# Kernel optimization log

Measured on AMD Instinct MI355X. Metric: run time of the kernel, lower is better.

Reference implementation:

```python
import jax, jax.numpy as jnp
import numpy as np

N = 50000      # nodes
E = 1_600_000  # edges
IN, HID, OUT, NC = 384, 128, 64, 2
EPS = 1e-5


def layer_norm(x, g, b):
    mu = x.mean(-1, keepdims=True)
    v = ((x - mu) ** 2).mean(-1, keepdims=True)
    return (x - mu) / jnp.sqrt(v + EPS) * g + b


def gat_conv(x, src, dst, ea, W, a_s, a_d, We, a_e, bias, n):
    """PyG GATConv, heads=1, edge_dim=1, add_self_loops with fill_value='mean'."""
    h = x @ W  # [n, F]
    # self-loop edge_attr = mean of incoming edge_attr per destination node
    ones = jnp.ones((src.shape[0],), h.dtype)
    cnt = jax.ops.segment_sum(ones, dst, num_segments=n)
    esum = jax.ops.segment_sum(ea, dst, num_segments=n)
    loop_ea = esum / jnp.maximum(cnt, 1.0)[:, None]
    loop = jnp.arange(n)
    s2 = jnp.concatenate([src, loop])
    d2 = jnp.concatenate([dst, loop])
    ea2 = jnp.concatenate([ea, loop_ea], axis=0)
    al_s = h @ a_s          # [n]
    al_d = h @ a_d          # [n]
    al_e = (ea2 @ We) @ a_e  # [E+n]
    logits = jax.nn.leaky_relu(al_s[s2] + al_d[d2] + al_e, 0.2)
    m = jax.ops.segment_max(logits, d2, num_segments=n)  # every node has a self loop
    ex = jnp.exp(logits - m[d2])
    den = jax.ops.segment_sum(ex, d2, num_segments=n)
    alpha = ex / den[d2]
    out = jax.ops.segment_sum(alpha[:, None] * h[s2], d2, num_segments=n)
    return out + bias


def setup_inputs() -> dict:
    key = jax.random.key(0)
    ks = jax.random.split(key, 20)
    def xav(k, fan_in, fan_out):
        s = float(np.sqrt(6.0 / (fan_in + fan_out)))
        return jax.random.uniform(k, (fan_in, fan_out), jnp.float32, -s, s)
    x = jax.random.normal(ks[0], (N, IN), jnp.float32)
    edge_index = jax.random.randint(ks[1], (2, E), 0, N)
    edge_attr = jax.random.normal(ks[2], (E, 1), jnp.float32)
    return {
        "x": x, "edge_index": edge_index, "edge_attr": edge_attr,
        "ln1_g": jnp.ones((IN,), jnp.float32), "ln1_b": jnp.zeros((IN,), jnp.float32),
        "fc1_w": xav(ks[3], IN, HID), "fc1_b": jnp.zeros((HID,), jnp.float32),
        "conv1_w": xav(ks[4], HID, HID),
        "conv1_as": jax.random.normal(ks[5], (HID,), jnp.float32) * 0.1,
        "conv1_ad": jax.random.normal(ks[6], (HID,), jnp.float32) * 0.1,
        "conv1_we": xav(ks[7], 1, HID),
        "conv1_ae": jax.random.normal(ks[8], (HID,), jnp.float32) * 0.1,
        "conv1_b": jnp.zeros((HID,), jnp.float32),
        "conv2_w": xav(ks[9], HID, OUT),
        "conv2_as": jax.random.normal(ks[10], (OUT,), jnp.float32) * 0.1,
        "conv2_ad": jax.random.normal(ks[11], (OUT,), jnp.float32) * 0.1,
        "conv2_we": xav(ks[12], 1, OUT),
        "conv2_ae": jax.random.normal(ks[13], (OUT,), jnp.float32) * 0.1,
        "conv2_b": jnp.zeros((OUT,), jnp.float32),
        "ln2_g": jnp.ones((OUT,), jnp.float32), "ln2_b": jnp.zeros((OUT,), jnp.float32),
        "fc2_w": xav(ks[14], OUT, NC), "fc2_b": jnp.zeros((NC,), jnp.float32),
    }


def reference(x, edge_index, edge_attr,
              ln1_g, ln1_b, fc1_w, fc1_b,
              conv1_w, conv1_as, conv1_ad, conv1_we, conv1_ae, conv1_b,
              conv2_w, conv2_as, conv2_ad, conv2_we, conv2_ae, conv2_b,
              ln2_g, ln2_b, fc2_w, fc2_b):
    src, dst = edge_index[0], edge_index[1]
    n = x.shape[0]
    h = layer_norm(x, ln1_g, ln1_b) @ fc1_w + fc1_b
    h = gat_conv(h, src, dst, edge_attr, conv1_w, conv1_as, conv1_ad, conv1_we, conv1_ae, conv1_b, n)
    h = jax.nn.leaky_relu(h, 0.01)
    h = gat_conv(h, src, dst, edge_attr, conv2_w, conv2_as, conv2_ad, conv2_we, conv2_ae, conv2_b, n)
    h = jax.nn.leaky_relu(h, 0.01)
    out = layer_norm(h, ln2_g, ln2_b) @ fc2_w + fc2_b
    return out
```

## Files before the change

### kernel.cpp

```cpp
#include <hip/hip_runtime.h>

#define NN 50000
#define NE 1600000
#define CAP 64
#define NBIN 196
#define NBLK 391
#define RUNCAP 48

typedef __attribute__((ext_vector_type(8))) short short8v;
typedef __attribute__((ext_vector_type(4))) float f32x4;

__device__ __forceinline__ float wsum(float v) {
#pragma unroll
  for (int m = 32; m > 0; m >>= 1) v += __shfl_xor(v, m, 64);
  return v;
}
__device__ __forceinline__ float wmax(float v) {
#pragma unroll
  for (int m = 32; m > 0; m >>= 1) v = fmaxf(v, __shfl_xor(v, m, 64));
  return v;
}
__device__ __forceinline__ float leakyf(float x, float s) { return x > 0.f ? x : s * x; }

__device__ __forceinline__ unsigned short bfr(float f) {
  unsigned u = __float_as_uint(f);
  return (unsigned short)((u + 0x7FFFu + ((u >> 16) & 1u)) >> 16);
}
__device__ __forceinline__ unsigned pack2(float a, float b) {
  return (unsigned)bfr(a) | ((unsigned)bfr(b) << 16);
}
__device__ __forceinline__ float bflo(unsigned u) { return __uint_as_float(u << 16); }
__device__ __forceinline__ float bfhi(unsigned u) { return __uint_as_float(u & 0xFFFF0000u); }

__global__ __launch_bounds__(256) void k_bin1(const int* __restrict__ src,
                                              const int* __restrict__ dst,
                                              const float* __restrict__ ea,
                                              int2* __restrict__ binRun,
                                              int* __restrict__ runLen) {
  __shared__ int cur[NBIN];
  int tid = threadIdx.x, b = blockIdx.x;
  for (int i = tid; i < NBIN; i += 256) cur[i] = 0;
  __syncthreads();
  int2* myRun = binRun + (size_t)b * NBIN * RUNCAP;
  int base4 = b * 1024;
#pragma unroll
  for (int i = 0; i < 4; ++i) {
    int t4 = base4 + i * 256 + tid;
    if (t4 < NE / 4) {
      int4 s = ((const int4*)src)[t4];
      int4 d = ((const int4*)dst)[t4];
      float4 a = ((const float4*)ea)[t4];
      int bin, p;
      bin = d.x >> 8; p = atomicAdd(&cur[bin], 1);
      if (p < RUNCAP) myRun[bin * RUNCAP + p] = make_int2(s.x | ((d.x & 255) << 16), __float_as_int(a.x));
      bin = d.y >> 8; p = atomicAdd(&cur[bin], 1);
      if (p < RUNCAP) myRun[bin * RUNCAP + p] = make_int2(s.y | ((d.y & 255) << 16), __float_as_int(a.y));
      bin = d.z >> 8; p = atomicAdd(&cur[bin], 1);
      if (p < RUNCAP) myRun[bin * RUNCAP + p] = make_int2(s.z | ((d.z & 255) << 16), __float_as_int(a.z));
      bin = d.w >> 8; p = atomicAdd(&cur[bin], 1);
      if (p < RUNCAP) myRun[bin * RUNCAP + p] = make_int2(s.w | ((d.w & 255) << 16), __float_as_int(a.w));
    }
  }
  __syncthreads();
  for (int i = tid; i < NBIN; i += 256) runLen[b * NBIN + i] = min(cur[i], RUNCAP);
}

__global__ __launch_bounds__(256) void k_bin2(const int2* __restrict__ binRun,
                                              const int* __restrict__ runLen,
                                              int2* __restrict__ edat, int* __restrict__ cnt) {
  __shared__ int cur[256];
  __shared__ int rl[NBLK];
  int tid = threadIdx.x, j = blockIdx.x;
  cur[tid] = 0;
  for (int i = tid; i < NBLK; i += 256) rl[i] = runLen[i * NBIN + j];
  __syncthreads();
  const int TOT = NBLK * RUNCAP;
  for (int g = tid; g < TOT; g += 256) {
    int b = g / RUNCAP, r = g - b * RUNCAP;
    if (r < rl[b]) {
      int2 rec = binRun[(size_t)b * NBIN * RUNCAP + j * RUNCAP + r];
      int srcv = rec.x & 0xFFFF;
      int dlow = rec.x >> 16;
      int dstv = (j << 8) | dlow;
      int p = atomicAdd(&cur[dlow], 1);
      if (p < CAP) edat[(size_t)dstv * CAP + p] = make_int2(srcv, rec.y);
    }
  }
  __syncthreads();
  int dstv = (j << 8) | tid;
  if (dstv < NN) cnt[dstv] = min(cur[tid], CAP);
}

__global__ void k_prep(const float* __restrict__ W, const float* __restrict__ g,
                       const float* __restrict__ b, const float* __restrict__ fb,
                       const float* __restrict__ we1, const float* __restrict__ ae1,
                       const float* __restrict__ we2, const float* __restrict__ ae2,
                       float* __restrict__ u, float* __restrict__ v, float* __restrict__ ce) {
  __shared__ float r1[128], r2[128];
  int c = threadIdx.x;
  float ua = 0.f, va = 0.f;
#pragma unroll 4
  for (int k = 0; k < 384; ++k) {
    float w = W[k * 128 + c];
    ua += g[k] * w;
    va += b[k] * w;
  }
  u[c] = ua;
  v[c] = va + fb[c];
  r1[c] = we1[c] * ae1[c];
  r2[c] = (c < 64) ? we2[c] * ae2[c] : 0.f;
  __syncthreads();
  for (int o = 64; o > 0; o >>= 1) {
    if (c < o) { r1[c] += r1[c + o]; r2[c] += r2[c + o]; }
    __syncthreads();
  }
  if (c == 0) { ce[0] = r1[0]; ce[1] = r2[0]; }
}

__global__ void k_prepT(const float* __restrict__ W1, const float* __restrict__ g,
                        const float* __restrict__ cw1, const float* __restrict__ cw2,
                        unsigned short* __restrict__ WgF, unsigned short* __restrict__ W1F,
                        unsigned short* __restrict__ W2F) {
  int tid = blockIdx.x * 256 + threadIdx.x;
  int stride = gridDim.x * 256;
  for (int i = tid; i < 8 * 12 * 512; i += stride) {
    int j = i & 7, lane = (i >> 3) & 63, tk = i >> 9;
    int ks = tk % 12, t = tk / 12;
    int c = t * 16 + (lane & 15);
    int k = ks * 32 + (lane >> 4) * 8 + j;
    WgF[i] = bfr(g[k] * W1[k * 128 + c]);
  }
  for (int i = tid; i < 8 * 4 * 512; i += stride) {
    int j = i & 7, lane = (i >> 3) & 63, tk = i >> 9;
    int ks = tk & 3, t = tk >> 2;
    int c = t * 16 + (lane & 15);
    int k = ks * 32 + (lane >> 4) * 8 + j;
    W1F[i] = bfr(cw1[k * 128 + c]);
  }
  for (int i = tid; i < 4 * 4 * 512; i += stride) {
    int j = i & 7, lane = (i >> 3) & 63, tk = i >> 9;
    int ks = tk & 3, t = tk >> 2;
    int c = t * 16 + (lane & 15);
    int k = ks * 32 + (lane >> 4) * 8 + j;
    W2F[i] = bfr(cw2[k * 64 + c]);
  }
}

__global__ __launch_bounds__(256) void k_fc1_h1(
    const float* __restrict__ x, const unsigned short* __restrict__ WgF,
    const unsigned short* __restrict__ W1F, const float* __restrict__ u,
    const float* __restrict__ v, const float* __restrict__ a_s,
    const float* __restrict__ a_d, unsigned short* __restrict__ Hb,
    float* __restrict__ al_s, float* __restrict__ al_d) {
  __shared__ __align__(16) unsigned short xs[64][392];
  __shared__ float mu_s[64], rs_s[64];
  int tid = threadIdx.x, wv = tid >> 6, lane = tid & 63;
  int lrow = lane & 15, lk = lane >> 4;
  long n0 = (long)blockIdx.x * 64;
  for (int rr = 0; rr < 16; ++rr) {
    int r = wv * 16 + rr;
    long gr = n0 + r;
    if (gr > NN - 1) gr = NN - 1;
    const float* xr = x + gr * 384;
    float s = 0.f, ss = 0.f;
#pragma unroll
    for (int js = 0; js < 3; ++js) {
      float2 val = *(const float2*)&xr[lane * 2 + 128 * js];
      s += val.x + val.y;
      ss += val.x * val.x + val.y * val.y;
      *(unsigned*)&xs[r][lane * 2 + 128 * js] = pack2(val.x, val.y);
    }
    s = wsum(s);
    ss = wsum(ss);
    if (lane == 0) {
      float mu = s * (1.f / 384.f);
      float var = ss * (1.f / 384.f) - mu * mu;
      mu_s[r] = mu;
      rs_s[r] = rsqrtf(var + 1e-5f);
    }
  }
  __syncthreads();
  const unsigned short* abase = &xs[wv * 16 + lrow][lk * 8];
  f32x4 acc[8] = {};
  for (int ks = 0; ks < 12; ++ks) {
    short8v A = *(const short8v*)(abase + ks * 32);
#pragma unroll
    for (int t = 0; t < 8; ++t) {
      short8v B = *(const short8v*)&WgF[((t * 12 + ks) * 64 + lane) * 8];
      acc[t] = __builtin_amdgcn_mfma_f32_16x16x32_bf16(A, B, acc[t], 0, 0, 0);
    }
  }
  float uc[8], vc[8];
#pragma unroll
  for (int t = 0; t < 8; ++t) {
    int c = t * 16 + lrow;
    uc[t] = u[c];
    vc[t] = v[c];
  }
#pragma unroll
  for (int reg = 0; reg < 4; ++reg) {
    int rl = wv * 16 + lk * 4 + reg;
    float mu = mu_s[rl], rs = rs_s[rl];
#pragma unroll
    for (int t = 0; t < 8; ++t) {
      float val = rs * (acc[t][reg] - mu * uc[t]) + vc[t];
      xs[rl][t * 16 + lrow] = bfr(val);
    }
  }
  __syncthreads();
  f32x4 acc2[8] = {};
#pragma unroll
  for (int ks = 0; ks < 4; ++ks) {
    short8v A = *(const short8v*)(abase + ks * 32);
#pragma unroll
    for (int t = 0; t < 8; ++t) {
      short8v B = *(const short8v*)&W1F[((t * 4 + ks) * 64 + lane) * 8];
      acc2[t] = __builtin_amdgcn_mfma_f32_16x16x32_bf16(A, B, acc2[t], 0, 0, 0);
    }
  }
  float asv[8], adv[8];
#pragma unroll
  for (int t = 0; t < 8; ++t) {
    asv[t] = a_s[t * 16 + lrow];
    adv[t] = a_d[t * 16 + lrow];
  }
#pragma unroll
  for (int reg = 0; reg < 4; ++reg) {
    float ps = 0.f, pd = 0.f;
#pragma unroll
    for (int t = 0; t < 8; ++t) {
      ps += acc2[t][reg] * asv[t];
      pd += acc2[t][reg] * adv[t];
    }
#pragma unroll
    for (int m = 1; m < 16; m <<= 1) {
      ps += __shfl_xor(ps, m, 64);
      pd += __shfl_xor(pd, m, 64);
    }
    long rg = n0 + wv * 16 + lk * 4 + reg;
    if (rg < NN) {
      if (lrow == 0) { al_s[rg] = ps; al_d[rg] = pd; }
#pragma unroll
      for (int t = 0; t < 8; ++t) Hb[rg * 128 + t * 16 + lrow] = bfr(acc2[t][reg]);
    }
  }
}

template <int NT>
__global__ __launch_bounds__(256) void k_mxw(
    const unsigned short* __restrict__ Xb, const unsigned short* __restrict__ WF,
    const float* __restrict__ a_s, const float* __restrict__ a_d,
    unsigned short* __restrict__ Hb, float* __restrict__ al_s, float* __restrict__ al_d) {
  __shared__ __align__(16) unsigned short xs[64][136];
  int tid = threadIdx.x, wv = tid >> 6, lane = tid & 63;
  int lrow = lane & 15, lk = lane >> 4;
  long n0 = (long)blockIdx.x * 64;
  for (int rr = 0; rr < 16; ++rr) {
    int r = wv * 16 + rr;
    long gr = n0 + r;
    if (gr > NN - 1) gr = NN - 1;
    *(unsigned*)&xs[r][lane * 2] = *(const unsigned*)&Xb[gr * 128 + lane * 2];
  }
  __syncthreads();
  const unsigned short* abase = &xs[wv * 16 + lrow][lk * 8];
  f32x4 acc[NT] = {};
#pragma unroll
  for (int ks = 0; ks < 4; ++ks) {
    short8v A = *(const short8v*)(abase + ks * 32);
#pragma unroll
    for (int t = 0; t < NT; ++t) {
      short8v B = *(const short8v*)&WF[((t * 4 + ks) * 64 + lane) * 8];
      acc[t] = __builtin_amdgcn_mfma_f32_16x16x32_bf16(A, B, acc[t], 0, 0, 0);
    }
  }
  float asv[NT], adv[NT];
#pragma unroll
  for (int t = 0; t < NT; ++t) {
    asv[t] = a_s[t * 16 + lrow];
    adv[t] = a_d[t * 16 + lrow];
  }
#pragma unroll
  for (int reg = 0; reg < 4; ++reg) {
    float ps = 0.f, pd = 0.f;
#pragma unroll
    for (int t = 0; t < NT; ++t) {
      ps += acc[t][reg] * asv[t];
      pd += acc[t][reg] * adv[t];
    }
#pragma unroll
    for (int m = 1; m < 16; m <<= 1) {
      ps += __shfl_xor(ps, m, 64);
      pd += __shfl_xor(pd, m, 64);
    }
    long rg = n0 + wv * 16 + lk * 4 + reg;
    if (rg < NN) {
      if (lrow == 0) { al_s[rg] = ps; al_d[rg] = pd; }
#pragma unroll
      for (int t = 0; t < NT; ++t) Hb[rg * (NT * 16) + t * 16 + lrow] = bfr(acc[t][reg]);
    }
  }
}

template <int F, bool OB, bool FUSE_LN>
__global__ __launch_bounds__(256) void k_agg(
    const unsigned short* __restrict__ Hb, const float* __restrict__ al_s,
    const float* __restrict__ al_d, const float* __restrict__ cep,
    const int* __restrict__ cntA, const int2* __restrict__ edat,
    const float* __restrict__ bias, void* __restrict__ outp,
    const float* __restrict__ g2, const float* __restrict__ b2,
    const float* __restrict__ w2, const float* __restrict__ fb2) {
  int wv = threadIdx.x >> 6, lane = threadIdx.x & 63;
  int i = blockIdx.x * 4 + wv;
  int cnt = min(cntA[i], CAP);
  float ce = *cep;
  float ald = al_d[i];
  bool valid = lane < cnt;
  int s = 0;
  float eav = 0.f, lg = -1e30f;
  if (valid) {
    int2 ed = edat[(size_t)i * CAP + lane];
    s = ed.x;
    eav = __int_as_float(ed.y);
    lg = leakyf(al_s[s] + ald + ce * eav, 0.2f);
  }
  float easum = wsum(eav);
  float loop_ea = easum / fmaxf((float)cnt, 1.f);
  float lg_self = leakyf(al_s[i] + ald + ce * loop_ea, 0.2f);
  float mx = fmaxf(wmax(lg), lg_self);
  float e = valid ? __expf(lg - mx) : 0.f;
  float es_ = __expf(lg_self - mx);
  float den = wsum(e) + es_;
  float acc0, acc1 = 0.f;
  if (F == 128) {
    unsigned u = *(const unsigned*)&Hb[(size_t)i * 128 + 2 * lane];
    acc0 = es_ * bflo(u);
    acc1 = es_ * bfhi(u);
  } else {
    acc0 = es_ * __uint_as_float(((unsigned)Hb[(size_t)i * 64 + lane]) << 16);
  }
  int t = 0;
  for (; t + 8 <= cnt; t += 8) {
    float et[8];
    unsigned uu[8];
#pragma unroll
    for (int j = 0; j < 8; ++j) {
      et[j] = __shfl(e, t + j, 64);
      int sj = __shfl(s, t + j, 64);
      if (F == 128)
        uu[j] = *(const unsigned*)&Hb[(size_t)sj * 128 + 2 * lane];
      else
        uu[j] = ((unsigned)Hb[(size_t)sj * 64 + lane]) << 16;
    }
#pragma unroll
    for (int j = 0; j < 8; ++j) {
      if (F == 128) {
        acc0 += et[j] * bflo(uu[j]);
        acc1 += et[j] * bfhi(uu[j]);
      } else {
        acc0 += et[j] * __uint_as_float(uu[j]);
      }
    }
  }
  for (; t < cnt; ++t) {
    float et = __shfl(e, t, 64);
    int st = __shfl(s, t, 64);
    if (F == 128) {
      unsigned u = *(const unsigned*)&Hb[(size_t)st * 128 + 2 * lane];
      acc0 += et * bflo(u);
      acc1 += et * bfhi(u);
    } else {
      acc0 += et * __uint_as_float(((unsigned)Hb[(size_t)st * 64 + lane]) << 16);
    }
  }
  float inv = 1.f / den;
  if (F == 128) {
    float2 bv = *(const float2*)&bias[2 * lane];
    float o0 = leakyf(acc0 * inv + bv.x, 0.01f);
    float o1 = leakyf(acc1 * inv + bv.y, 0.01f);
    if (OB) {
      ((unsigned*)outp)[(size_t)i * 64 + lane] = pack2(o0, o1);
    } else {
      *(float2*)&((float*)outp)[(size_t)i * 128 + 2 * lane] = make_float2(o0, o1);
    }
  } else {
    float o = leakyf(acc0 * inv + bias[lane], 0.01f);
    if (FUSE_LN) {
      float sum = wsum(o);
      float ssum = wsum(o * o);
      float mu = sum * (1.f / 64.f);
      float var = ssum * (1.f / 64.f) - mu * mu;
      float rs = rsqrtf(var + 1e-5f);
      float xn = (o - mu) * rs * g2[lane] + b2[lane];
      float q0 = wsum(xn * w2[lane * 2 + 0]);
      float q1 = wsum(xn * w2[lane * 2 + 1]);
      if (lane == 0) {
        ((float*)outp)[(size_t)i * 2 + 0] = q0 + fb2[0];
        ((float*)outp)[(size_t)i * 2 + 1] = q1 + fb2[1];
      }
    } else {
      ((float*)outp)[(size_t)i * 64 + lane] = o;
    }
  }
}

extern "C" void kernel_launch(void* const* d_in, const int* in_sizes, int n_in,
                              void* d_out, int out_size, void* d_ws, size_t ws_size,
                              hipStream_t stream) {
  const int N = NN;
  const float* x = (const float*)d_in[0];
  const int* ei = (const int*)d_in[1];
  const float* ea = (const float*)d_in[2];
  const float* ln1_g = (const float*)d_in[3];
  const float* ln1_b = (const float*)d_in[4];
  const float* fc1_w = (const float*)d_in[5];
  const float* fc1_b = (const float*)d_in[6];
  const float* c1_w = (const float*)d_in[7];
  const float* c1_as = (const float*)d_in[8];
  const float* c1_ad = (const float*)d_in[9];
  const float* c1_we = (const float*)d_in[10];
  const float* c1_ae = (const float*)d_in[11];
  const float* c1_b = (const float*)d_in[12];
  const float* c2_w = (const float*)d_in[13];
  const float* c2_as = (const float*)d_in[14];
  const float* c2_ad = (const float*)d_in[15];
  const float* c2_we = (const float*)d_in[16];
  const float* c2_ae = (const float*)d_in[17];
  const float* c2_b = (const float*)d_in[18];
  const float* ln2_g = (const float*)d_in[19];
  const float* ln2_b = (const float*)d_in[20];
  const float* fc2_w = (const float*)d_in[21];
  const float* fc2_b = (const float*)d_in[22];

  const int* src = ei;
  const int* dst = ei + NE;

  unsigned short* spare = (unsigned short*)d_ws;
  unsigned short* Hb = spare + (size_t)N * 128;
  unsigned short* o1b = Hb + (size_t)N * 128;
  float* al_s = (float*)(o1b + (size_t)N * 128);
  float* al_d = al_s + N;
  float* cebuf = al_d + N;
  float* uvec = cebuf + 4;
  float* vvec = uvec + 128;
  unsigned short* WgF = (unsigned short*)(vvec + 128);
  unsigned short* W1F = WgF + 8 * 12 * 512;
  unsigned short* W2F = W1F + 8 * 4 * 512;
  int* cnt = (int*)(W2F + 4 * 4 * 512);
  int* runLen = cnt + N;
  int2* edat = (int2*)((((uintptr_t)(runLen + NBLK * NBIN)) + 15) & ~(uintptr_t)15);
  int2* binRun = (int2*)d_ws;

  size_t need = ((char*)(edat + (size_t)N * CAP)) - (char*)d_ws;
  if (ws_size < need) return;

  k_bin1<<<NBLK, 256, 0, stream>>>(src, dst, ea, binRun, runLen);
  k_bin2<<<NBIN, 256, 0, stream>>>(binRun, runLen, edat, cnt);
  k_prep<<<1, 128, 0, stream>>>(fc1_w, ln1_g, ln1_b, fc1_b, c1_we, c1_ae, c2_we, c2_ae,
                                uvec, vvec, cebuf);
  k_prepT<<<64, 256, 0, stream>>>(fc1_w, ln1_g, c1_w, c2_w, WgF, W1F, W2F);

  k_fc1_h1<<<(N + 63) / 64, 256, 0, stream>>>(x, WgF, W1F, uvec, vvec, c1_as, c1_ad,
                                              Hb, al_s, al_d);
  k_agg<128, true, false><<<N / 4, 256, 0, stream>>>(Hb, al_s, al_d, cebuf + 0, cnt, edat,
                                                     c1_b, o1b, nullptr, nullptr, nullptr,
                                                     nullptr);

  k_mxw<4><<<(N + 63) / 64, 256, 0, stream>>>(o1b, W2F, c2_as, c2_ad, Hb, al_s, al_d);
  k_agg<64, false, true><<<N / 4, 256, 0, stream>>>(Hb, al_s, al_d, cebuf + 1, cnt, edat,
                                                    c2_b, d_out, ln2_g, ln2_b, fc2_w, fc2_b);
}
```

Baseline: 250.4 us.

## Split each node's edge aggregation across two wavefronts with shared-memory reduction

The GAT aggregation kernel now gives each destination node two wavefronts. Each wavefront handles alternating incoming edges, so the serial gather loop per wavefront is about half as long. Partial max, edge-attr sums, denominators and feature accumulators are combined through shared memory with two block barriers, and the grid doubles. The intent is to shorten the latency-bound gather chain and raise memory-level parallelism, at the cost of extra syncs, LDS traffic and twice as many waves per node.

```diff
diff --git a/kernel.cpp b/kernel.cpp
--- a/kernel.cpp
+++ b/kernel.cpp
@@ -309,37 +309,52 @@
     const float* __restrict__ bias, void* __restrict__ outp,
     const float* __restrict__ g2, const float* __restrict__ b2,
     const float* __restrict__ w2, const float* __restrict__ fb2) {
-  int wv = threadIdx.x >> 6, lane = threadIdx.x & 63;
-  int i = blockIdx.x * 4 + wv;
+  __shared__ float sh_acc[2][128];
+  __shared__ float sh_ea[2][2], sh_mx[2][2], sh_den[2];
+  int tid = threadIdx.x, wv = tid >> 6, lane = tid & 63;
+  int nloc = wv >> 1, half = wv & 1;
+  int i = blockIdx.x * 2 + nloc;
   int cnt = min(cntA[i], CAP);
   float ce = *cep;
   float ald = al_d[i];
-  bool valid = lane < cnt;
+  int myc = (cnt + 1 - half) >> 1;
+  bool valid = lane < myc;
   int s = 0;
   float eav = 0.f, lg = -1e30f;
   if (valid) {
-    int2 ed = edat[(size_t)i * CAP + lane];
+    int2 ed = edat[(size_t)i * CAP + 2 * lane + half];
     s = ed.x;
     eav = __int_as_float(ed.y);
     lg = leakyf(al_s[s] + ald + ce * eav, 0.2f);
   }
-  float easum = wsum(eav);
+  float ea_p = wsum(eav);
+  float mx_p = wmax(lg);
+  if (lane == 0) {
+    sh_ea[nloc][half] = ea_p;
+    sh_mx[nloc][half] = mx_p;
+  }
+  __syncthreads();
+  float easum = sh_ea[nloc][0] + sh_ea[nloc][1];
+  float mxn = fmaxf(sh_mx[nloc][0], sh_mx[nloc][1]);
   float loop_ea = easum / fmaxf((float)cnt, 1.f);
   float lg_self = leakyf(al_s[i] + ald + ce * loop_ea, 0.2f);
-  float mx = fmaxf(wmax(lg), lg_self);
+  float mx = fmaxf(mxn, lg_self);
   float e = valid ? __expf(lg - mx) : 0.f;
   float es_ = __expf(lg_self - mx);
-  float den = wsum(e) + es_;
-  float acc0, acc1 = 0.f;
-  if (F == 128) {
-    unsigned u = *(const unsigned*)&Hb[(size_t)i * 128 + 2 * lane];
-    acc0 = es_ * bflo(u);
-    acc1 = es_ * bfhi(u);
-  } else {
-    acc0 = es_ * __uint_as_float(((unsigned)Hb[(size_t)i * 64 + lane]) << 16);
+  float den_p = wsum(e);
+  float acc0 = 0.f, acc1 = 0.f;
+  if (half == 0) {
+    den_p += es_;
+    if (F == 128) {
+      unsigned u = *(const unsigned*)&Hb[(size_t)i * 128 + 2 * lane];
+      acc0 = es_ * bflo(u);
+      acc1 = es_ * bfhi(u);
+    } else {
+      acc0 = es_ * __uint_as_float(((unsigned)Hb[(size_t)i * 64 + lane]) << 16);
+    }
   }
   int t = 0;
-  for (; t + 8 <= cnt; t += 8) {
+  for (; t + 8 <= myc; t += 8) {
     float et[8];
     unsigned uu[8];
 #pragma unroll
@@ -361,7 +376,7 @@
       }
     }
   }
-  for (; t < cnt; ++t) {
+  for (; t < myc; ++t) {
     float et = __shfl(e, t, 64);
     int st = __shfl(s, t, 64);
     if (F == 128) {
@@ -372,33 +387,52 @@
       acc0 += et * __uint_as_float(((unsigned)Hb[(size_t)st * 64 + lane]) << 16);
     }
   }
-  float inv = 1.f / den;
-  if (F == 128) {
-    float2 bv = *(const float2*)&bias[2 * lane];
-    float o0 = leakyf(acc0 * inv + bv.x, 0.01f);
-    float o1 = leakyf(acc1 * inv + bv.y, 0.01f);
-    if (OB) {
-      ((unsigned*)outp)[(size_t)i * 64 + lane] = pack2(o0, o1);
+  if (half == 1) {
+    if (F == 128) {
+      sh_acc[nloc][2 * lane] = acc0;
+      sh_acc[nloc][2 * lane + 1] = acc1;
     } else {
-      *(float2*)&((float*)outp)[(size_t)i * 128 + 2 * lane] = make_float2(o0, o1);
-    }
-  } else {
-    float o = leakyf(acc0 * inv + bias[lane], 0.01f);
-    if (FUSE_LN) {
-      float sum = wsum(o);
-      float ssum = wsum(o * o);
-      float mu = sum * (1.f / 64.f);
-      float var = ssum * (1.f / 64.f) - mu * mu;
-      float rs = rsqrtf(var + 1e-5f);
-      float xn = (o - mu) * rs * g2[lane] + b2[lane];
-      float q0 = wsum(xn * w2[lane * 2 + 0]);
-      float q1 = wsum(xn * w2[lane * 2 + 1]);
-      if (lane == 0) {
-        ((float*)outp)[(size_t)i * 2 + 0] = q0 + fb2[0];
-        ((float*)outp)[(size_t)i * 2 + 1] = q1 + fb2[1];
+      sh_acc[nloc][lane] = acc0;
+    }
+    if (lane == 0) sh_den[nloc] = den_p;
+  }
+  __syncthreads();
+  if (half == 0) {
+    float den = den_p + sh_den[nloc];
+    if (F == 128) {
+      acc0 += sh_acc[nloc][2 * lane];
+      acc1 += sh_acc[nloc][2 * lane + 1];
+    } else {
+      acc0 += sh_acc[nloc][lane];
+    }
+    float inv = 1.f / den;
+    if (F == 128) {
+      float2 bv = *(const float2*)&bias[2 * lane];
+      float o0 = leakyf(acc0 * inv + bv.x, 0.01f);
+      float o1 = leakyf(acc1 * inv + bv.y, 0.01f);
+      if (OB) {
+        ((unsigned*)outp)[(size_t)i * 64 + lane] = pack2(o0, o1);
+      } else {
+        *(float2*)&((float*)outp)[(size_t)i * 128 + 2 * lane] = make_float2(o0, o1);
       }
     } else {
-      ((float*)outp)[(size_t)i * 64 + lane] = o;
+      float o = leakyf(acc0 * inv + bias[lane], 0.01f);
+      if (FUSE_LN) {
+        float sum = wsum(o);
+        float ssum = wsum(o * o);
+        float mu = sum * (1.f / 64.f);
+        float var = ssum * (1.f / 64.f) - mu * mu;
+        float rs = rsqrtf(var + 1e-5f);
+        float xn = (o - mu) * rs * g2[lane] + b2[lane];
+        float q0 = wsum(xn * w2[lane * 2 + 0]);
+        float q1 = wsum(xn * w2[lane * 2 + 1]);
+        if (lane == 0) {
+          ((float*)outp)[(size_t)i * 2 + 0] = q0 + fb2[0];
+          ((float*)outp)[(size_t)i * 2 + 1] = q1 + fb2[1];
+        }
+      } else {
+        ((float*)outp)[(size_t)i * 64 + lane] = o;
+      }
     }
   }
 }
@@ -461,11 +495,11 @@
 
   k_fc1_h1<<<(N + 63) / 64, 256, 0, stream>>>(x, WgF, W1F, uvec, vvec, c1_as, c1_ad,
                                               Hb, al_s, al_d);
-  k_agg<128, true, false><<<N / 4, 256, 0, stream>>>(Hb, al_s, al_d, cebuf + 0, cnt, edat,
+  k_agg<128, true, false><<<N / 2, 256, 0, stream>>>(Hb, al_s, al_d, cebuf + 0, cnt, edat,
                                                      c1_b, o1b, nullptr, nullptr, nullptr,
                                                      nullptr);
 
   k_mxw<4><<<(N + 63) / 64, 256, 0, stream>>>(o1b, W2F, c2_as, c2_ad, Hb, al_s, al_d);
-  k_agg<64, false, true><<<N / 4, 256, 0, stream>>>(Hb, al_s, al_d, cebuf + 1, cnt, edat,
+  k_agg<64, false, true><<<N / 2, 256, 0, stream>>>(Hb, al_s, al_d, cebuf + 1, cnt, edat,
                                                     c2_b, d_out, ln2_g, ln2_b, fc2_w, fc2_b);
 }
```

Result: slower. 289.9 us (+15.8%).

## Merge prep and binning kernels so independent stages run in one launch

Applied to the files above, without the earlier changes.

Folds the four preparation kernels into two launches. k_pre1 runs edge binning pass 1, the weight repacking and the u/v/ce reductions in disjoint block ranges. k_main1 runs binning pass 2 alongside the fc1/conv1 projection blocks, reusing the projection's shared memory for the bin counters. binRun moves to its own workspace region so it no longer aliases buffers written concurrently. The intent is to cut launch overhead and overlap independent stages; the cost is a larger workspace and uneven block workloads within each merged launch.

```diff
diff --git a/kernel.cpp b/kernel.cpp
--- a/kernel.cpp
+++ b/kernel.cpp
@@ -6,6 +6,7 @@
 #define NBIN 196
 #define NBLK 391
 #define RUNCAP 48
+#define FC1B 782
 
 typedef __attribute__((ext_vector_type(8))) short short8v;
 typedef __attribute__((ext_vector_type(4))) float f32x4;
@@ -32,131 +33,132 @@
 __device__ __forceinline__ float bflo(unsigned u) { return __uint_as_float(u << 16); }
 __device__ __forceinline__ float bfhi(unsigned u) { return __uint_as_float(u & 0xFFFF0000u); }
 
-__global__ __launch_bounds__(256) void k_bin1(const int* __restrict__ src,
-                                              const int* __restrict__ dst,
-                                              const float* __restrict__ ea,
-                                              int2* __restrict__ binRun,
-                                              int* __restrict__ runLen) {
+__global__ __launch_bounds__(256) void k_pre1(
+    const int* __restrict__ src, const int* __restrict__ dst, const float* __restrict__ ea,
+    int2* __restrict__ binRun, int* __restrict__ runLen,
+    const float* __restrict__ fc1w, const float* __restrict__ g, const float* __restrict__ b,
+    const float* __restrict__ fb, const float* __restrict__ we1, const float* __restrict__ ae1,
+    const float* __restrict__ we2, const float* __restrict__ ae2,
+    const float* __restrict__ cw1, const float* __restrict__ cw2,
+    unsigned short* __restrict__ WgF, unsigned short* __restrict__ W1F,
+    unsigned short* __restrict__ W2F, float* __restrict__ u, float* __restrict__ v,
+    float* __restrict__ ce) {
   __shared__ int cur[NBIN];
-  int tid = threadIdx.x, b = blockIdx.x;
-  for (int i = tid; i < NBIN; i += 256) cur[i] = 0;
-  __syncthreads();
-  int2* myRun = binRun + (size_t)b * NBIN * RUNCAP;
-  int base4 = b * 1024;
-#pragma unroll
-  for (int i = 0; i < 4; ++i) {
-    int t4 = base4 + i * 256 + tid;
-    if (t4 < NE / 4) {
-      int4 s = ((const int4*)src)[t4];
-      int4 d = ((const int4*)dst)[t4];
-      float4 a = ((const float4*)ea)[t4];
-      int bin, p;
-      bin = d.x >> 8; p = atomicAdd(&cur[bin], 1);
-      if (p < RUNCAP) myRun[bin * RUNCAP + p] = make_int2(s.x | ((d.x & 255) << 16), __float_as_int(a.x));
-      bin = d.y >> 8; p = atomicAdd(&cur[bin], 1);
-      if (p < RUNCAP) myRun[bin * RUNCAP + p] = make_int2(s.y | ((d.y & 255) << 16), __float_as_int(a.y));
-      bin = d.z >> 8; p = atomicAdd(&cur[bin], 1);
-      if (p < RUNCAP) myRun[bin * RUNCAP + p] = make_int2(s.z | ((d.z & 255) << 16), __float_as_int(a.z));
-      bin = d.w >> 8; p = atomicAdd(&cur[bin], 1);
-      if (p < RUNCAP) myRun[bin * RUNCAP + p] = make_int2(s.w | ((d.w & 255) << 16), __float_as_int(a.w));
-    }
-  }
-  __syncthreads();
-  for (int i = tid; i < NBIN; i += 256) runLen[b * NBIN + i] = min(cur[i], RUNCAP);
-}
-
-__global__ __launch_bounds__(256) void k_bin2(const int2* __restrict__ binRun,
-                                              const int* __restrict__ runLen,
-                                              int2* __restrict__ edat, int* __restrict__ cnt) {
-  __shared__ int cur[256];
-  __shared__ int rl[NBLK];
-  int tid = threadIdx.x, j = blockIdx.x;
-  cur[tid] = 0;
-  for (int i = tid; i < NBLK; i += 256) rl[i] = runLen[i * NBIN + j];
-  __syncthreads();
-  const int TOT = NBLK * RUNCAP;
-  for (int g = tid; g < TOT; g += 256) {
-    int b = g / RUNCAP, r = g - b * RUNCAP;
-    if (r < rl[b]) {
-      int2 rec = binRun[(size_t)b * NBIN * RUNCAP + j * RUNCAP + r];
-      int srcv = rec.x & 0xFFFF;
-      int dlow = rec.x >> 16;
-      int dstv = (j << 8) | dlow;
-      int p = atomicAdd(&cur[dlow], 1);
-      if (p < CAP) edat[(size_t)dstv * CAP + p] = make_int2(srcv, rec.y);
-    }
-  }
-  __syncthreads();
-  int dstv = (j << 8) | tid;
-  if (dstv < NN) cnt[dstv] = min(cur[tid], CAP);
-}
-
-__global__ void k_prep(const float* __restrict__ W, const float* __restrict__ g,
-                       const float* __restrict__ b, const float* __restrict__ fb,
-                       const float* __restrict__ we1, const float* __restrict__ ae1,
-                       const float* __restrict__ we2, const float* __restrict__ ae2,
-                       float* __restrict__ u, float* __restrict__ v, float* __restrict__ ce) {
   __shared__ float r1[128], r2[128];
-  int c = threadIdx.x;
-  float ua = 0.f, va = 0.f;
+  int tid = threadIdx.x, bid = blockIdx.x;
+  if (bid < NBLK) {
+    for (int i = tid; i < NBIN; i += 256) cur[i] = 0;
+    __syncthreads();
+    int2* myRun = binRun + (size_t)bid * NBIN * RUNCAP;
+    int base4 = bid * 1024;
+#pragma unroll
+    for (int i = 0; i < 4; ++i) {
+      int t4 = base4 + i * 256 + tid;
+      if (t4 < NE / 4) {
+        int4 s = ((const int4*)src)[t4];
+        int4 d = ((const int4*)dst)[t4];
+        float4 a = ((const float4*)ea)[t4];
+        int bin, p;
+        bin = d.x >> 8; p = atomicAdd(&cur[bin], 1);
+        if (p < RUNCAP) myRun[bin * RUNCAP + p] = make_int2(s.x | ((d.x & 255) << 16), __float_as_int(a.x));
+        bin = d.y >> 8; p = atomicAdd(&cur[bin], 1);
+        if (p < RUNCAP) myRun[bin * RUNCAP + p] = make_int2(s.y | ((d.y & 255) << 16), __float_as_int(a.y));
+        bin = d.z >> 8; p = atomicAdd(&cur[bin], 1);
+        if (p < RUNCAP) myRun[bin * RUNCAP + p] = make_int2(s.z | ((d.z & 255) << 16), __float_as_int(a.z));
+        bin = d.w >> 8; p = atomicAdd(&cur[bin], 1);
+        if (p < RUNCAP) myRun[bin * RUNCAP + p] = make_int2(s.w | ((d.w & 255) << 16), __float_as_int(a.w));
+      }
+    }
+    __syncthreads();
+    for (int i = tid; i < NBIN; i += 256) runLen[bid * NBIN + i] = min(cur[i], RUNCAP);
+  } else if (bid < NBLK + 64) {
+    int vb = bid - NBLK;
+    int t0 = vb * 256 + tid;
+    const int stride = 64 * 256;
+    for (int i = t0; i < 8 * 12 * 512; i += stride) {
+      int j = i & 7, lane = (i >> 3) & 63, tk = i >> 9;
+      int ks = tk % 12, t = tk / 12;
+      int c = t * 16 + (lane & 15);
+      int k = ks * 32 + (lane >> 4) * 8 + j;
+      WgF[i] = bfr(g[k] * fc1w[k * 128 + c]);
+    }
+    for (int i = t0; i < 8 * 4 * 512; i += stride) {
+      int j = i & 7, lane = (i >> 3) & 63, tk = i >> 9;
+      int ks = tk & 3, t = tk >> 2;
+      int c = t * 16 + (lane & 15);
+      int k = ks * 32 + (lane >> 4) * 8 + j;
+      W1F[i] = bfr(cw1[k * 128 + c]);
+    }
+    for (int i = t0; i < 4 * 4 * 512; i += stride) {
+      int j = i & 7, lane = (i >> 3) & 63, tk = i >> 9;
+      int ks = tk & 3, t = tk >> 2;
+      int c = t * 16 + (lane & 15);
+      int k = ks * 32 + (lane >> 4) * 8 + j;
+      W2F[i] = bfr(cw2[k * 64 + c]);
+    }
+  } else {
+    int c = tid;
+    if (c < 128) {
+      float ua = 0.f, va = 0.f;
 #pragma unroll 4
-  for (int k = 0; k < 384; ++k) {
-    float w = W[k * 128 + c];
-    ua += g[k] * w;
-    va += b[k] * w;
-  }
-  u[c] = ua;
-  v[c] = va + fb[c];
-  r1[c] = we1[c] * ae1[c];
-  r2[c] = (c < 64) ? we2[c] * ae2[c] : 0.f;
-  __syncthreads();
-  for (int o = 64; o > 0; o >>= 1) {
-    if (c < o) { r1[c] += r1[c + o]; r2[c] += r2[c + o]; }
+      for (int k = 0; k < 384; ++k) {
+        float w = fc1w[k * 128 + c];
+        ua += g[k] * w;
+        va += b[k] * w;
+      }
+      u[c] = ua;
+      v[c] = va + fb[c];
+      r1[c] = we1[c] * ae1[c];
+      r2[c] = (c < 64) ? we2[c] * ae2[c] : 0.f;
+    }
     __syncthreads();
-  }
-  if (c == 0) { ce[0] = r1[0]; ce[1] = r2[0]; }
-}
-
-__global__ void k_prepT(const float* __restrict__ W1, const float* __restrict__ g,
-                        const float* __restrict__ cw1, const float* __restrict__ cw2,
-                        unsigned short* __restrict__ WgF, unsigned short* __restrict__ W1F,
-                        unsigned short* __restrict__ W2F) {
-  int tid = blockIdx.x * 256 + threadIdx.x;
-  int stride = gridDim.x * 256;
-  for (int i = tid; i < 8 * 12 * 512; i += stride) {
-    int j = i & 7, lane = (i >> 3) & 63, tk = i >> 9;
-    int ks = tk % 12, t = tk / 12;
-    int c = t * 16 + (lane & 15);
-    int k = ks * 32 + (lane >> 4) * 8 + j;
-    WgF[i] = bfr(g[k] * W1[k * 128 + c]);
-  }
-  for (int i = tid; i < 8 * 4 * 512; i += stride) {
-    int j = i & 7, lane = (i >> 3) & 63, tk = i >> 9;
-    int ks = tk & 3, t = tk >> 2;
-    int c = t * 16 + (lane & 15);
-    int k = ks * 32 + (lane >> 4) * 8 + j;
-    W1F[i] = bfr(cw1[k * 128 + c]);
-  }
-  for (int i = tid; i < 4 * 4 * 512; i += stride) {
-    int j = i & 7, lane = (i >> 3) & 63, tk = i >> 9;
-    int ks = tk & 3, t = tk >> 2;
-    int c = t * 16 + (lane & 15);
-    int k = ks * 32 + (lane >> 4) * 8 + j;
-    W2F[i] = bfr(cw2[k * 64 + c]);
-  }
-}
-
-__global__ __launch_bounds__(256) void k_fc1_h1(
+    for (int o = 64; o > 0; o >>= 1) {
+      if (c < o) { r1[c] += r1[c + o]; r2[c] += r2[c + o]; }
+      __syncthreads();
+    }
+    if (c == 0) { ce[0] = r1[0]; ce[1] = r2[0]; }
+  }
+}
+
+__global__ __launch_bounds__(256) void k_main1(
     const float* __restrict__ x, const unsigned short* __restrict__ WgF,
     const unsigned short* __restrict__ W1F, const float* __restrict__ u,
     const float* __restrict__ v, const float* __restrict__ a_s,
     const float* __restrict__ a_d, unsigned short* __restrict__ Hb,
-    float* __restrict__ al_s, float* __restrict__ al_d) {
+    float* __restrict__ al_s, float* __restrict__ al_d,
+    const int2* __restrict__ binRun, const int* __restrict__ runLen,
+    int2* __restrict__ edat, int* __restrict__ cnt) {
   __shared__ __align__(16) unsigned short xs[64][392];
   __shared__ float mu_s[64], rs_s[64];
-  int tid = threadIdx.x, wv = tid >> 6, lane = tid & 63;
+  int tid = threadIdx.x, bid = blockIdx.x;
+  if (bid < NBIN) {
+    int j = bid;
+    int* cur = (int*)&xs[0][0];
+    int* rl = cur + 256;
+    cur[tid] = 0;
+    for (int i = tid; i < NBLK; i += 256) rl[i] = runLen[i * NBIN + j];
+    __syncthreads();
+    const int TOT = NBLK * RUNCAP;
+    for (int g = tid; g < TOT; g += 256) {
+      int b = g / RUNCAP, r = g - b * RUNCAP;
+      if (r < rl[b]) {
+        int2 rec = binRun[(size_t)b * NBIN * RUNCAP + j * RUNCAP + r];
+        int srcv = rec.x & 0xFFFF;
+        int dlow = rec.x >> 16;
+        int dstv = (j << 8) | dlow;
+        int p = atomicAdd(&cur[dlow], 1);
+        if (p < CAP) edat[(size_t)dstv * CAP + p] = make_int2(srcv, rec.y);
+      }
+    }
+    __syncthreads();
+    int dstv = (j << 8) | tid;
+    if (dstv < NN) cnt[dstv] = min(cur[tid], CAP);
+    return;
+  }
+  int fb1 = bid - NBIN;
+  int wv = tid >> 6, lane = tid & 63;
   int lrow = lane & 15, lk = lane >> 4;
-  long n0 = (long)blockIdx.x * 64;
+  long n0 = (long)fb1 * 64;
   for (int rr = 0; rr < 16; ++rr) {
     int r = wv * 16 + rr;
     long gr = n0 + r;
@@ -199,12 +201,12 @@
   }
 #pragma unroll
   for (int reg = 0; reg < 4; ++reg) {
-    int rl = wv * 16 + lk * 4 + reg;
-    float mu = mu_s[rl], rs = rs_s[rl];
+    int rl2 = wv * 16 + lk * 4 + reg;
+    float mu = mu_s[rl2], rs = rs_s[rl2];
 #pragma unroll
     for (int t = 0; t < 8; ++t) {
       float val = rs * (acc[t][reg] - mu * uc[t]) + vc[t];
-      xs[rl][t * 16 + lrow] = bfr(val);
+      xs[rl2][t * 16 + lrow] = bfr(val);
     }
   }
   __syncthreads();
@@ -448,24 +450,22 @@
   int* cnt = (int*)(W2F + 4 * 4 * 512);
   int* runLen = cnt + N;
   int2* edat = (int2*)((((uintptr_t)(runLen + NBLK * NBIN)) + 15) & ~(uintptr_t)15);
-  int2* binRun = (int2*)d_ws;
-
-  size_t need = ((char*)(edat + (size_t)N * CAP)) - (char*)d_ws;
+  int2* binRun = (int2*)(edat + (size_t)N * CAP);
+
+  size_t need = ((char*)(binRun + (size_t)NBLK * NBIN * RUNCAP)) - (char*)d_ws;
   if (ws_size < need) return;
 
-  k_bin1<<<NBLK, 256, 0, stream>>>(src, dst, ea, binRun, runLen);
-  k_bin2<<<NBIN, 256, 0, stream>>>(binRun, runLen, edat, cnt);
-  k_prep<<<1, 128, 0, stream>>>(fc1_w, ln1_g, ln1_b, fc1_b, c1_we, c1_ae, c2_we, c2_ae,
-                                uvec, vvec, cebuf);
-  k_prepT<<<64, 256, 0, stream>>>(fc1_w, ln1_g, c1_w, c2_w, WgF, W1F, W2F);
-
-  k_fc1_h1<<<(N + 63) / 64, 256, 0, stream>>>(x, WgF, W1F, uvec, vvec, c1_as, c1_ad,
-                                              Hb, al_s, al_d);
+  k_pre1<<<NBLK + 64 + 1, 256, 0, stream>>>(src, dst, ea, binRun, runLen,
+                                            fc1_w, ln1_g, ln1_b, fc1_b,
+                                            c1_we, c1_ae, c2_we, c2_ae, c1_w, c2_w,
+                                            WgF, W1F, W2F, uvec, vvec, cebuf);
+  k_main1<<<NBIN + FC1B, 256, 0, stream>>>(x, WgF, W1F, uvec, vvec, c1_as, c1_ad,
+                                           Hb, al_s, al_d, binRun, runLen, edat, cnt);
+
   k_agg<128, true, false><<<N / 4, 256, 0, stream>>>(Hb, al_s, al_d, cebuf + 0, cnt, edat,
                                                      c1_b, o1b, nullptr, nullptr, nullptr,
                                                      nullptr);
-
-  k_mxw<4><<<(N + 63) / 64, 256, 0, stream>>>(o1b, W2F, c2_as, c2_ad, Hb, al_s, al_d);
+  k_mxw<4><<<FC1B, 256, 0, stream>>>(o1b, W2F, c2_as, c2_ad, Hb, al_s, al_d);
   k_agg<64, false, true><<<N / 4, 256, 0, stream>>>(Hb, al_s, al_d, cebuf + 1, cnt, edat,
                                                     c2_b, d_out, ln2_g, ln2_b, fc2_w, fc2_b);
 }
```

After: 207.4 us. 1.21x faster.
